# Kernel optimization log

Measured on AMD Instinct MI355X. Metric: run time of the kernel, lower is better.

The kernel has to match this reference:

```python
import jax, jax.numpy as jnp
import numpy as np

N_HEADS = 16
HEAD_DIM = 64
EMB = 1024
B, S = 2, 2048


def setup_inputs() -> dict:
    key = jax.random.key(0)
    ks = jax.random.split(key, 8)
    inner = N_HEADS * HEAD_DIM
    return {
        "query": jax.random.normal(ks[0], (B, S, EMB), dtype=jnp.float32),
        "key": jax.random.normal(ks[1], (B, S, EMB), dtype=jnp.float32),
        "value": jax.random.normal(ks[2], (B, S, EMB), dtype=jnp.float32),
        "positional_mask": jnp.ones((B, S), dtype=bool),
        "future_mask": 1,
        # torch nn.Linear weight layout: (out_features, in_features)
        "Wq": jax.random.normal(ks[3], (inner, EMB), dtype=jnp.float32) * 0.02,
        "Wk": jax.random.normal(ks[4], (inner, EMB), dtype=jnp.float32) * 0.02,
        "Wv": jax.random.normal(ks[5], (inner, EMB), dtype=jnp.float32) * 0.02,
        "Wo": jax.random.normal(ks[6], (EMB, inner), dtype=jnp.float32) * 0.02,
        "bo": jax.random.normal(ks[7], (EMB,), dtype=jnp.float32) * 0.02,
    }


def reference(query, key, value, positional_mask, future_mask, Wq, Wk, Wv, Wo, bo):
    batch, seq = query.shape[:2]
    # project and split heads: (B, S, H, D)
    q = (query @ Wq.T).reshape(batch, seq, N_HEADS, HEAD_DIM)
    k = (key @ Wk.T).reshape(batch, seq, N_HEADS, HEAD_DIM)
    v = (value @ Wv.T).reshape(batch, seq, N_HEADS, HEAD_DIM)
    scale = 1.0 / np.sqrt(HEAD_DIM).astype(np.float32)
    # (B, H, Sq, Sk)
    weights = jnp.einsum("bqhd,bkhd->bhqk", q, k) * scale
    neg_inf = jnp.float32(-jnp.inf)
    # additive key-position mask
    reweight = jnp.where(positional_mask, jnp.float32(0.0), neg_inf)  # (B, S)
    weights = weights + reweight[:, None, None, :]
    if future_mask:
        causal = jnp.triu(jnp.full((seq, seq), neg_inf, dtype=weights.dtype), k=1)
        weights = weights + causal
    weights = jax.nn.softmax(weights, axis=-1)
    out = jnp.einsum("bhqk,bkhd->bqhd", weights, v).reshape(batch, seq, -1)
    return out @ Wo.T + bo
```

## Files before the change

### kernel.cpp

```cpp
#include <hip/hip_runtime.h>
#include <hip/hip_bf16.h>
#include <math.h>

#define EMB    1024
#define NH     16
#define HD     64
#define BATCH  2
#define SEQ    2048
#define MTOK   (BATCH * SEQ)

typedef __bf16 bf16_t;
typedef __bf16 bf16x8 __attribute__((ext_vector_type(8)));
typedef __bf16 bf16x4 __attribute__((ext_vector_type(4)));
typedef float  f32x4  __attribute__((ext_vector_type(4)));

#define NEG_BIG (-1.0e30f)

#define GLD16(g, l) __builtin_amdgcn_global_load_lds(                     \
    (const __attribute__((address_space(1))) void*)(g),                   \
    (__attribute__((address_space(3))) void*)(l), 16, 0, 0)

__device__ inline bf16x8 ld_frag64(const bf16_t* __restrict__ p) {
    const bf16x4 lo = *(const bf16x4*)p;
    const bf16x4 hi = *(const bf16x4*)(p + 4);
    bf16x8 r;
#pragma unroll
    for (int j = 0; j < 4; ++j) { r[j] = lo[j]; r[j + 4] = hi[j]; }
    return r;
}

__global__ __launch_bounds__(256) void cast_bf16(
    const float* __restrict__ q, const float* __restrict__ k,
    const float* __restrict__ v, const float* __restrict__ wq,
    const float* __restrict__ wk, const float* __restrict__ wv,
    const float* __restrict__ wo, bf16_t* __restrict__ ws)
{
    const size_t g = ((size_t)blockIdx.x * 256 + threadIdx.x) * 8;
    const size_t BIG = (size_t)1 << 22;
    const size_t SML = (size_t)1 << 20;
    const float* src;
    bf16_t* dst;
    size_t off;
    if (g < 3 * BIG) {
        const int s = (int)(g >> 22);
        src = s == 0 ? q : (s == 1 ? k : v);
        dst = ws + (size_t)s * BIG;
        off = g & (BIG - 1);
    } else {
        const size_t h = g - 3 * BIG;
        const int s = (int)(h >> 20);
        src = s == 0 ? wq : (s == 1 ? wk : (s == 2 ? wv : wo));
        dst = ws + 3 * BIG + (size_t)s * SML;
        off = h & (SML - 1);
    }
    const f32x4 f0 = *(const f32x4*)(src + off);
    const f32x4 f1 = *(const f32x4*)(src + off + 4);
    bf16x8 r;
#pragma unroll
    for (int j = 0; j < 4; ++j) { r[j] = (bf16_t)f0[j]; r[j + 4] = (bf16_t)f1[j]; }
    *(bf16x8*)(dst + off) = r;
}

__global__ __launch_bounds__(512) void gemm_qkv(
    const bf16_t* __restrict__ A0, const bf16_t* __restrict__ W0,
    bf16_t* __restrict__ Cp, size_t sA, size_t sW, size_t sC, float ascale)
{
    constexpr int K = EMB, N = EMB;
    __shared__ __align__(16) bf16_t As[2][256 * 64];
    __shared__ __align__(16) bf16_t Bs[2][256 * 64];

    const int tid  = threadIdx.x;
    const int wave = tid >> 6;
    const int lane = tid & 63;
    const int l15  = lane & 15;
    const int quad = lane >> 4;

    const int bid = blockIdx.x;
    const int wg  = (bid & 7) * 24 + (bid >> 3);
    const int y   = wg & 15;
    const int pan = wg >> 4;
    const int x   = pan & 3;
    const int z   = pan >> 2;

    const bf16_t* A  = A0 + (size_t)z * sA;
    const bf16_t* Wb = W0 + (size_t)z * sW;
    const int m0 = y * 256, n0 = x * 256;
    const int wm = (wave >> 2) * 128;
    const int wn = (wave & 3) * 64;

    const int srow = lane >> 3;
    const int scol = ((lane & 7) ^ srow) * 8;
    const bf16_t* gA = A  + (size_t)(m0 + wave * 32 + srow) * K + scol;
    const bf16_t* gB = Wb + (size_t)(n0 + wave * 32 + srow) * K + scol;
    const int loff = wave * 32 * 64;

    f32x4 acc[8][4] = {};

    auto stage = [&](int t, int b) {
        const size_t ko = (size_t)t * 64;
#pragma unroll
        for (int i = 0; i < 4; ++i) {
            GLD16(gA + ko + (size_t)i * 8 * K, &As[b][loff + i * 512]);
            GLD16(gB + ko + (size_t)i * 8 * K, &Bs[b][loff + i * 512]);
        }
    };

    stage(0, 0);

    for (int t = 0; t < 16; ++t) {
        const int cur = t & 1;
        __builtin_amdgcn_s_barrier();
        if (t + 1 < 16) {
            stage(t + 1, cur ^ 1);
            asm volatile("s_waitcnt vmcnt(8)" ::: "memory");
        } else {
            asm volatile("s_waitcnt vmcnt(0)" ::: "memory");
        }
        __builtin_amdgcn_s_barrier();

#pragma unroll
        for (int h = 0; h < 2; ++h) {
            bf16x8 af[8], bfr[4];
#pragma unroll
            for (int mt = 0; mt < 8; ++mt) {
                const int r = wm + mt * 16 + l15;
                const int c8 = (quad + h * 4) ^ (l15 & 7);
                af[mt] = *(const bf16x8*)&As[cur][r * 64 + c8 * 8];
            }
#pragma unroll
            for (int nt = 0; nt < 4; ++nt) {
                const int r = wn + nt * 16 + l15;
                const int c8 = (quad + h * 4) ^ (l15 & 7);
                bfr[nt] = *(const bf16x8*)&Bs[cur][r * 64 + c8 * 8];
            }
            __builtin_amdgcn_s_setprio(1);
#pragma unroll
            for (int mt = 0; mt < 8; ++mt)
#pragma unroll
                for (int nt = 0; nt < 4; ++nt)
                    acc[mt][nt] = __builtin_amdgcn_mfma_f32_16x16x32_bf16(
                        af[mt], bfr[nt], acc[mt][nt], 0, 0, 0);
            __builtin_amdgcn_s_setprio(0);
        }
    }

    bf16_t* C = Cp + (size_t)z * sC;
    const float sc = (z == 0) ? ascale : 1.0f;
#pragma unroll
    for (int nt = 0; nt < 4; ++nt) {
        const int col = n0 + wn + nt * 16 + l15;
#pragma unroll
        for (int mt = 0; mt < 8; ++mt) {
#pragma unroll
            for (int r = 0; r < 4; ++r) {
                const int row = m0 + wm + mt * 16 + quad * 4 + r;
                C[(size_t)row * N + col] = (bf16_t)(acc[mt][nt][r] * sc);
            }
        }
    }
}

__global__ __launch_bounds__(256) void gemm_wo(
    const bf16_t* __restrict__ A, const bf16_t* __restrict__ Wb,
    const float* __restrict__ bias, float* __restrict__ Cp)
{
    constexpr int K = EMB, N = EMB;
    constexpr int nT = K / 32;
    __shared__ __align__(16) bf16_t As[3][128 * 32];
    __shared__ __align__(16) bf16_t Bs[3][128 * 32];

    const int tid  = threadIdx.x;
    const int wave = tid >> 6;
    const int lane = tid & 63;
    const int l15  = lane & 15;
    const int quad = lane >> 4;

    const int m0 = blockIdx.y * 128;
    const int n0 = blockIdx.x * 128;
    const int wm = (wave >> 1) * 64;
    const int wn = (wave & 1) * 64;

    const int lrow = lane >> 2;
    const int scol = ((lane & 3) ^ (lrow & 3)) * 8;
    const bf16_t* gA = A  + (size_t)(m0 + wave * 32 + lrow) * K + scol;
    const bf16_t* gB = Wb + (size_t)(n0 + wave * 32 + lrow) * K + scol;
    const int loff = wave * 1024;

    f32x4 acc[4][4] = {};
    const int xq = (quad ^ (l15 & 3)) * 8;

    auto stage = [&](int t, int b3) {
        const size_t ko = (size_t)t * 32;
        GLD16(gA + ko, &As[b3][loff]);
        GLD16(gA + ko + (size_t)16 * K, &As[b3][loff + 512]);
        GLD16(gB + ko, &Bs[b3][loff]);
        GLD16(gB + ko + (size_t)16 * K, &Bs[b3][loff + 512]);
    };

    stage(0, 0);
    stage(1, 1);

    int cur = 0;
    for (int t = 0; t < nT; ++t) {
        if (t == nT - 1) asm volatile("s_waitcnt vmcnt(0)" ::: "memory");
        else             asm volatile("s_waitcnt vmcnt(4)" ::: "memory");
        __builtin_amdgcn_s_barrier();

        bf16x8 af[4], bfr[4];
#pragma unroll
        for (int mt = 0; mt < 4; ++mt)
            af[mt] = *(const bf16x8*)&As[cur][(wm + mt * 16 + l15) * 32 + xq];
#pragma unroll
        for (int nt = 0; nt < 4; ++nt)
            bfr[nt] = *(const bf16x8*)&Bs[cur][(wn + nt * 16 + l15) * 32 + xq];
        __builtin_amdgcn_s_setprio(1);
#pragma unroll
        for (int mt = 0; mt < 4; ++mt)
#pragma unroll
            for (int nt = 0; nt < 4; ++nt)
                acc[mt][nt] = __builtin_amdgcn_mfma_f32_16x16x32_bf16(
                    af[mt], bfr[nt], acc[mt][nt], 0, 0, 0);
        __builtin_amdgcn_s_setprio(0);

        if (t + 2 < nT) {
            int b3 = cur + 2; if (b3 >= 3) b3 -= 3;
            stage(t + 2, b3);
        }
        if (++cur == 3) cur = 0;
    }

#pragma unroll
    for (int nt = 0; nt < 4; ++nt) {
        const int col = n0 + wn + nt * 16 + l15;
        const float bv = bias[col];
#pragma unroll
        for (int mt = 0; mt < 4; ++mt)
#pragma unroll
            for (int r = 0; r < 4; ++r) {
                const int row = m0 + wm + mt * 16 + quad * 4 + r;
                Cp[(size_t)row * N + col] = acc[mt][nt][r] + bv;
            }
    }
}

__global__ __launch_bounds__(256) void attn_flash(
    const bf16_t* __restrict__ Q, const bf16_t* __restrict__ Km,
    const bf16_t* __restrict__ V, bf16_t* __restrict__ O)
{
    __shared__ __align__(16) bf16_t Ks[2][64 * 64];
    __shared__ __align__(16) bf16_t Vs[2][64][76];
    __shared__ bf16_t Pb[4][16 * 68];
    __shared__ bf16_t Ob[4][16 * 72];

    const int tid  = threadIdx.x;
    const int wave = tid >> 6;
    const int lane = tid & 63;
    const int l15  = lane & 15;
    const int quad = lane >> 4;
    const int b = blockIdx.z, h = blockIdx.y;

    const bf16_t* Qb = Q  + ((size_t)b * SEQ) * EMB + h * HD;
    const bf16_t* Kb = Km + ((size_t)b * SEQ) * EMB + h * HD;
    const bf16_t* Vb = V  + ((size_t)b * SEQ) * EMB + h * HD;

    const int krow = lane >> 3;
    const int kcol = ((lane & 7) ^ krow) * 8;
    const int vk   = wave * 16;
    const int vrow = lane >> 3;
    const int vd   = (lane & 7) * 8;
    bf16_t* P = Pb[wave];
    const int sw = l15 & 7;

    for (int ph = 0; ph < 2; ++ph) {
        const int qi = (ph == 0) ? (int)blockIdx.x : 31 - (int)blockIdx.x;
        const int qbase = qi * 64 + wave * 16;
        const int qg = qbase + l15;
        const int nkt = qi + 1;

        const bf16x8 qlo = *(const bf16x8*)(Qb + (size_t)(qbase + l15) * EMB + quad * 8);
        const bf16x8 qhi = *(const bf16x8*)(Qb + (size_t)(qbase + l15) * EMB + 32 + quad * 8);

        float m_s = NEG_BIG, l_s = 0.0f;
        f32x4 o[4] = {};

        __syncthreads();
#pragma unroll
        for (int i = 0; i < 2; ++i) {
            const int r0 = wave * 16 + i * 8;
            GLD16(Kb + (size_t)(r0 + krow) * EMB + kcol, &Ks[0][r0 * 64]);
        }
        {
            const bf16x8 v0 = *(const bf16x8*)(Vb + (size_t)(vk + vrow) * EMB + vd);
            const bf16x8 v1 = *(const bf16x8*)(Vb + (size_t)(vk + 8 + vrow) * EMB + vd);
            const int kr = vk + vrow;
#pragma unroll
            for (int j = 0; j < 8; ++j) Vs[0][vd + j][kr]     = v0[j];
#pragma unroll
            for (int j = 0; j < 8; ++j) Vs[0][vd + j][kr + 8] = v1[j];
        }

        for (int kt = 0; kt < nkt; ++kt) {
            const int cur = kt & 1, nb = cur ^ 1;
            const int kb = kt * 64;
            __syncthreads();

            bf16x8 v0, v1;
            const bool more = (kt + 1) < nkt;
            if (more) {
                const int kb1 = kb + 64;
#pragma unroll
                for (int i = 0; i < 2; ++i) {
                    const int r0 = wave * 16 + i * 8;
                    GLD16(Kb + (size_t)(kb1 + r0 + krow) * EMB + kcol, &Ks[nb][r0 * 64]);
                }
                v0 = *(const bf16x8*)(Vb + (size_t)(kb1 + vk + vrow) * EMB + vd);
                v1 = *(const bf16x8*)(Vb + (size_t)(kb1 + vk + 8 + vrow) * EMB + vd);
            }

            f32x4 s[4];
            __builtin_amdgcn_s_setprio(1);
#pragma unroll
            for (int t2 = 0; t2 < 4; ++t2) {
                const int row = t2 * 16 + l15;
                const bf16x8 klo = *(const bf16x8*)&Ks[cur][row * 64 + ((quad ^ sw) * 8)];
                const bf16x8 khi = *(const bf16x8*)&Ks[cur][row * 64 + (((4 + quad) ^ sw) * 8)];
                f32x4 a = {};
                a = __builtin_amdgcn_mfma_f32_16x16x32_bf16(klo, qlo, a, 0, 0, 0);
                a = __builtin_amdgcn_mfma_f32_16x16x32_bf16(khi, qhi, a, 0, 0, 0);
                s[t2] = a;
            }
            __builtin_amdgcn_s_setprio(0);

            if (more) {
                const int kr = vk + vrow;
#pragma unroll
                for (int j = 0; j < 8; ++j) Vs[nb][vd + j][kr]     = v0[j];
#pragma unroll
                for (int j = 0; j < 8; ++j) Vs[nb][vd + j][kr + 8] = v1[j];
            }

            float sc[16];
#pragma unroll
            for (int t2 = 0; t2 < 4; ++t2)
#pragma unroll
                for (int r = 0; r < 4; ++r)
                    sc[t2 * 4 + r] = s[t2][r];
            if (kt == nkt - 1) {
#pragma unroll
                for (int t2 = 0; t2 < 4; ++t2)
#pragma unroll
                    for (int r = 0; r < 4; ++r)
                        if (kb + t2 * 16 + quad * 4 + r > qg)
                            sc[t2 * 4 + r] = NEG_BIG;
            }
            const float a0 = fmaxf(fmaxf(sc[0],  sc[1]),  sc[2]);
            const float a1 = fmaxf(fmaxf(sc[3],  sc[4]),  sc[5]);
            const float a2 = fmaxf(fmaxf(sc[6],  sc[7]),  sc[8]);
            const float a3 = fmaxf(fmaxf(sc[9],  sc[10]), sc[11]);
            const float a4 = fmaxf(fmaxf(sc[12], sc[13]), sc[14]);
            float mx = fmaxf(fmaxf(fmaxf(fmaxf(a0, a1), a2), fmaxf(a3, a4)), sc[15]);
            mx = fmaxf(mx, __shfl_xor(mx, 16, 64));
            mx = fmaxf(mx, __shfl_xor(mx, 32, 64));
            if (!__all(mx - m_s <= 11.5f)) {
                const float mnew  = fmaxf(m_s, mx);
                const float alpha = __builtin_amdgcn_exp2f(m_s - mnew);
                l_s *= alpha;
#pragma unroll
                for (int dt = 0; dt < 4; ++dt)
#pragma unroll
                    for (int r = 0; r < 4; ++r) o[dt][r] *= alpha;
                m_s = mnew;
            }
            float e[16], rs = 0.0f;
#pragma unroll
            for (int j = 0; j < 16; ++j) {
                e[j] = __builtin_amdgcn_exp2f(sc[j] - m_s);
                rs += e[j];
            }
            rs += __shfl_xor(rs, 16, 64);
            rs += __shfl_xor(rs, 32, 64);
            l_s += rs;

#pragma unroll
            for (int t2 = 0; t2 < 4; ++t2) {
                bf16x4 p4;
#pragma unroll
                for (int r = 0; r < 4; ++r) p4[r] = (bf16_t)e[t2 * 4 + r];
                *(bf16x4*)&P[l15 * 68 + t2 * 16 + quad * 4] = p4;
            }
            __asm__ volatile("s_waitcnt lgkmcnt(0)" ::: "memory");
            const bf16x8 pb0 = ld_frag64(&P[l15 * 68 + quad * 8]);
            const bf16x8 pb1 = ld_frag64(&P[l15 * 68 + 32 + quad * 8]);

            __builtin_amdgcn_s_setprio(1);
#pragma unroll
            for (int dt = 0; dt < 4; ++dt) {
                const bf16x8 va0 = ld_frag64(&Vs[cur][dt * 16 + l15][quad * 8]);
                const bf16x8 va1 = ld_frag64(&Vs[cur][dt * 16 + l15][32 + quad * 8]);
                o[dt] = __builtin_amdgcn_mfma_f32_16x16x32_bf16(va0, pb0, o[dt], 0, 0, 0);
                o[dt] = __builtin_amdgcn_mfma_f32_16x16x32_bf16(va1, pb1, o[dt], 0, 0, 0);
            }
            __builtin_amdgcn_s_setprio(0);
        }

        const float inv = 1.0f / l_s;
        bf16_t* OT = Ob[wave];
#pragma unroll
        for (int dt = 0; dt < 4; ++dt) {
            bf16x4 pk;
#pragma unroll
            for (int r = 0; r < 4; ++r) pk[r] = (bf16_t)(o[dt][r] * inv);
            *(bf16x4*)&OT[l15 * 72 + dt * 16 + quad * 4] = pk;
        }
        __asm__ volatile("s_waitcnt lgkmcnt(0)" ::: "memory");
        const bf16x8 r0 = *(const bf16x8*)&OT[l15 * 72 + quad * 16];
        const bf16x8 r1 = *(const bf16x8*)&OT[l15 * 72 + quad * 16 + 8];
        bf16_t* dst = O + ((size_t)b * SEQ + qbase + l15) * EMB + h * HD + quad * 16;
        *(bf16x8*)dst       = r0;
        *(bf16x8*)(dst + 8) = r1;
    }
}

extern "C" void kernel_launch(void* const* d_in, const int* in_sizes, int n_in,
                              void* d_out, int out_size, void* d_ws, size_t ws_size,
                              hipStream_t stream)
{
    const float* query = (const float*)d_in[0];
    const float* key   = (const float*)d_in[1];
    const float* value = (const float*)d_in[2];
    const float* Wq = (const float*)d_in[5];
    const float* Wk = (const float*)d_in[6];
    const float* Wv = (const float*)d_in[7];
    const float* Wo = (const float*)d_in[8];
    const float* bo = (const float*)d_in[9];

    const size_t BIG = (size_t)1 << 22, SML = (size_t)1 << 20;
    bf16_t* ws  = (bf16_t*)d_ws;
    bf16_t* qc  = ws;
    bf16_t* kc  = qc + BIG;
    bf16_t* vc  = kc + BIG;
    bf16_t* wqc = vc + BIG;
    bf16_t* wkc = wqc + SML;
    bf16_t* wvc = wkc + SML;
    bf16_t* woc = wvc + SML;
    bf16_t* Qp  = woc + SML;
    bf16_t* Kp  = Qp + BIG;
    bf16_t* Vp  = Kp + BIG;
    bf16_t* Ab  = Vp + BIG;

    const dim3 blk(256);
    const float QSCALE = 0.18033688011112042f;

    cast_bf16<<<dim3(8192), blk, 0, stream>>>(query, key, value, Wq, Wk, Wv, Wo, ws);

    gemm_qkv<<<dim3(192), dim3(512), 0, stream>>>(
        qc, wqc, Qp, BIG, SML, BIG, QSCALE);

    attn_flash<<<dim3(SEQ / 128, NH, BATCH), blk, 0, stream>>>(Qp, Kp, Vp, Ab);

    gemm_wo<<<dim3(EMB / 128, MTOK / 128), blk, 0, stream>>>(
        Ab, woc, bo, (float*)d_out);
    (void)kc; (void)vc;
}
```

Baseline: 236.2 us.

## Deepen QKV GEMM pipeline to four-stage K=32 ring with single barrier

Restructures the QKV projection GEMM's shared-memory pipeline from a two-buffer, K=64 step into a four-buffer ring of K=32 slices, prefetching three stages ahead. It uses one barrier per iteration instead of two, with counted vmcnt waits. The LDS swizzle and the global-to-LDS load mapping are redone to fit the 32-wide rows. The aim is to hide more global-load latency behind MFMA work. The cost is twice as many loop iterations with smaller compute per barrier, and tighter correctness around the wait counts.

```diff
diff --git a/kernel.cpp b/kernel.cpp
--- a/kernel.cpp
+++ b/kernel.cpp
@@ -66,8 +66,9 @@
     bf16_t* __restrict__ Cp, size_t sA, size_t sW, size_t sC, float ascale)
 {
     constexpr int K = EMB, N = EMB;
-    __shared__ __align__(16) bf16_t As[2][256 * 64];
-    __shared__ __align__(16) bf16_t Bs[2][256 * 64];
+    constexpr int nS = K / 32;
+    __shared__ __align__(16) bf16_t As[4][256 * 32];
+    __shared__ __align__(16) bf16_t Bs[4][256 * 32];
 
     const int tid  = threadIdx.x;
     const int wave = tid >> 6;
@@ -88,60 +89,55 @@
     const int wm = (wave >> 2) * 128;
     const int wn = (wave & 3) * 64;
 
-    const int srow = lane >> 3;
-    const int scol = ((lane & 7) ^ srow) * 8;
-    const bf16_t* gA = A  + (size_t)(m0 + wave * 32 + srow) * K + scol;
-    const bf16_t* gB = Wb + (size_t)(n0 + wave * 32 + srow) * K + scol;
-    const int loff = wave * 32 * 64;
+    const int srow = tid >> 2;
+    const int scol = ((tid & 3) ^ ((srow >> 1) & 3)) * 8;
+    const bf16_t* gA0 = A  + (size_t)(m0 + srow) * K + scol;
+    const bf16_t* gA1 = A  + (size_t)(m0 + 128 + srow) * K + scol;
+    const bf16_t* gB0 = Wb + (size_t)(n0 + srow) * K + scol;
+    const bf16_t* gB1 = Wb + (size_t)(n0 + 128 + srow) * K + scol;
+    const int ldsw = wave * 512;
 
     f32x4 acc[8][4] = {};
-
-    auto stage = [&](int t, int b) {
-        const size_t ko = (size_t)t * 64;
-#pragma unroll
-        for (int i = 0; i < 4; ++i) {
-            GLD16(gA + ko + (size_t)i * 8 * K, &As[b][loff + i * 512]);
-            GLD16(gB + ko + (size_t)i * 8 * K, &Bs[b][loff + i * 512]);
-        }
+    const int cswz = (l15 >> 1) & 3;
+
+    auto stage = [&](int s) {
+        const int b = s & 3;
+        const size_t ko = (size_t)s * 32;
+        GLD16(gA0 + ko, &As[b][ldsw]);
+        GLD16(gA1 + ko, &As[b][4096 + ldsw]);
+        GLD16(gB0 + ko, &Bs[b][ldsw]);
+        GLD16(gB1 + ko, &Bs[b][4096 + ldsw]);
     };
 
-    stage(0, 0);
-
-    for (int t = 0; t < 16; ++t) {
-        const int cur = t & 1;
-        __builtin_amdgcn_s_barrier();
-        if (t + 1 < 16) {
-            stage(t + 1, cur ^ 1);
-            asm volatile("s_waitcnt vmcnt(8)" ::: "memory");
-        } else {
-            asm volatile("s_waitcnt vmcnt(0)" ::: "memory");
-        }
-        __builtin_amdgcn_s_barrier();
-
-#pragma unroll
-        for (int h = 0; h < 2; ++h) {
-            bf16x8 af[8], bfr[4];
-#pragma unroll
-            for (int mt = 0; mt < 8; ++mt) {
-                const int r = wm + mt * 16 + l15;
-                const int c8 = (quad + h * 4) ^ (l15 & 7);
-                af[mt] = *(const bf16x8*)&As[cur][r * 64 + c8 * 8];
-            }
-#pragma unroll
-            for (int nt = 0; nt < 4; ++nt) {
-                const int r = wn + nt * 16 + l15;
-                const int c8 = (quad + h * 4) ^ (l15 & 7);
-                bfr[nt] = *(const bf16x8*)&Bs[cur][r * 64 + c8 * 8];
-            }
-            __builtin_amdgcn_s_setprio(1);
-#pragma unroll
-            for (int mt = 0; mt < 8; ++mt)
-#pragma unroll
-                for (int nt = 0; nt < 4; ++nt)
-                    acc[mt][nt] = __builtin_amdgcn_mfma_f32_16x16x32_bf16(
-                        af[mt], bfr[nt], acc[mt][nt], 0, 0, 0);
-            __builtin_amdgcn_s_setprio(0);
-        }
+    stage(0); stage(1); stage(2);
+    asm volatile("s_waitcnt vmcnt(8)" ::: "memory");
+    __builtin_amdgcn_s_barrier();
+
+    for (int s = 0; s < nS; ++s) {
+        if (s + 3 < nS) stage(s + 3);
+        const int b = s & 3;
+        bf16x8 af[8], bfr[4];
+#pragma unroll
+        for (int mt = 0; mt < 8; ++mt)
+            af[mt] = *(const bf16x8*)&As[b][(wm + mt * 16 + l15) * 32 + ((quad ^ cswz) * 8)];
+#pragma unroll
+        for (int nt = 0; nt < 4; ++nt)
+            bfr[nt] = *(const bf16x8*)&Bs[b][(wn + nt * 16 + l15) * 32 + ((quad ^ cswz) * 8)];
+        asm volatile("s_waitcnt lgkmcnt(0)" ::: "memory");
+        __builtin_amdgcn_sched_barrier(0);
+        __builtin_amdgcn_s_setprio(1);
+#pragma unroll
+        for (int mt = 0; mt < 8; ++mt)
+#pragma unroll
+            for (int nt = 0; nt < 4; ++nt)
+                acc[mt][nt] = __builtin_amdgcn_mfma_f32_16x16x32_bf16(
+                    af[mt], bfr[nt], acc[mt][nt], 0, 0, 0);
+        __builtin_amdgcn_s_setprio(0);
+
+        if (s < nS - 3)       asm volatile("s_waitcnt vmcnt(8)" ::: "memory");
+        else if (s == nS - 3) asm volatile("s_waitcnt vmcnt(4)" ::: "memory");
+        else if (s == nS - 2) asm volatile("s_waitcnt vmcnt(0)" ::: "memory");
+        if (s < nS - 1) __builtin_amdgcn_s_barrier();
     }
 
     bf16_t* C = Cp + (size_t)z * sC;
```

Result: slower. 243.6 us (+3.1%).
